# Performance work log

Measured on AMD Instinct MI355X. Metric: run time of the kernel, lower is better.

Reference implementation:

```python
import jax, jax.numpy as jnp
import numpy as np

N = 4096
D = 1024          # latent_vector_size
H, KD, VD = 16, 64, 64
MHK = H * KD      # 1024
MHV = H * VD      # 1024
HID = D // 2      # 512
EPS = 1e-5


def _layernorm(v, g, b):
    mu = jnp.mean(v, axis=-1, keepdims=True)
    var = jnp.mean(jnp.square(v - mu), axis=-1, keepdims=True)
    return (v - mu) * jax.lax.rsqrt(var + EPS) * g + b


def setup_inputs() -> dict:
    key = jax.random.key(0)
    ks = jax.random.split(key, 12)
    s = lambda fan_in: 1.0 / np.sqrt(fan_in)
    return {
        "x": jax.random.normal(ks[0], (N, D), dtype=jnp.float32),
        "w_qkv": jax.random.uniform(ks[1], (D, H * (2 * KD + VD)), jnp.float32, -s(D), s(D)),
        "b_qkv": jax.random.uniform(ks[2], (H * (2 * KD + VD),), jnp.float32, -s(D), s(D)),
        "w_msa": jax.random.uniform(ks[3], (MHV, D), jnp.float32, -s(MHV), s(MHV)),
        "b_msa": jax.random.uniform(ks[4], (D,), jnp.float32, -s(MHV), s(MHV)),
        "ln_g": jnp.ones((D,), jnp.float32),
        "ln_b": jnp.zeros((D,), jnp.float32),
        "w_h1": jax.random.uniform(ks[5], (D, HID), jnp.float32, -s(D), s(D)),
        "b_h1": jax.random.uniform(ks[6], (HID,), jnp.float32, -s(D), s(D)),
        "w_h2": jax.random.uniform(ks[7], (HID, D), jnp.float32, -s(HID), s(HID)),
        "b_h2": jax.random.uniform(ks[8], (D,), jnp.float32, -s(HID), s(HID)),
    }


def reference(x, w_qkv, b_qkv, w_msa, b_msa, ln_g, ln_b, w_h1, b_h1, w_h2, b_h2):
    # --- attention block (note: heads are never split; one big [N,N] softmax) ---
    ln1 = _layernorm(x, ln_g, ln_b)                       # [N, D]
    qkv = ln1 @ w_qkv + b_qkv                             # [N, 3*MHK]
    q, k, v = qkv[:, :MHK], qkv[:, MHK:2 * MHK], qkv[:, 2 * MHK:]
    scores = (q @ k.T) / jnp.sqrt(jnp.float32(KD))        # [N, N]
    attn = jax.nn.softmax(scores, axis=-1)
    mha = (attn @ v) @ w_msa + b_msa                      # [N, D]
    enc1 = x + mha
    # --- MLP block (shared layernorm params; softmax output, residual) ---
    ln2 = _layernorm(enc1, ln_g, ln_b)
    h1 = jax.nn.gelu(ln2 @ w_h1 + b_h1, approximate=False)  # [N, HID]
    h2 = jax.nn.gelu(h1 @ w_h2 + b_h2, approximate=False)   # [N, D]
    out = jax.nn.softmax(h2, axis=-1)                        # nn.Softmax() -> dim=1 for 2D
    return enc1 + out
```

## Files before the change

### kernel.cpp

```cpp
#include <hip/hip_runtime.h>
#include <stdint.h>

#define DEV __device__ __forceinline__

typedef unsigned short u16;
typedef __attribute__((ext_vector_type(8))) unsigned short u16x8;
typedef __attribute__((ext_vector_type(4))) unsigned short u16x4;
typedef __attribute__((ext_vector_type(4))) float f32x4;

DEV float bf2f(u16 u) { return __uint_as_float(((unsigned)u) << 16); }
DEV u16 f2bf(float f) {
  unsigned u = __float_as_uint(f);
  u += 0x7FFFu + ((u >> 16) & 1u);
  return (u16)(u >> 16);
}
DEV float gelu_exact(float v) { return 0.5f * v * (1.0f + erff(v * 0.70710678118654752f)); }

__global__ __launch_bounds__(256) void transpose_f32_bf16(
    const float* __restrict__ in, u16* __restrict__ out, int rows, int cols) {
  __shared__ float t[32][33];
  const int tx = threadIdx.x, ty = threadIdx.y;
  const int c0 = blockIdx.x * 32, r0 = blockIdx.y * 32;
#pragma unroll
  for (int i = 0; i < 32; i += 8) t[ty + i][tx] = in[(size_t)(r0 + ty + i) * cols + c0 + tx];
  __syncthreads();
#pragma unroll
  for (int i = 0; i < 32; i += 8)
    out[(size_t)(c0 + ty + i) * rows + r0 + tx] = f2bf(t[tx][ty + i]);
}

__global__ __launch_bounds__(256) void transpose_bf16(
    const u16* __restrict__ in, int ldin, u16* __restrict__ out, int ldout) {
  __shared__ u16 t[32][33];
  const int tx = threadIdx.x, ty = threadIdx.y;
  const int c0 = blockIdx.x * 32, r0 = blockIdx.y * 32;
#pragma unroll
  for (int i = 0; i < 32; i += 8) t[ty + i][tx] = in[(size_t)(r0 + ty + i) * ldin + c0 + tx];
  __syncthreads();
#pragma unroll
  for (int i = 0; i < 32; i += 8)
    out[(size_t)(c0 + ty + i) * ldout + r0 + tx] = t[tx][ty + i];
}

__global__ __launch_bounds__(256) void layernorm_bf16(
    const float* __restrict__ in, const float* __restrict__ g,
    const float* __restrict__ b, u16* __restrict__ out) {
  const int tid = threadIdx.x;
  const int lane = tid & 63, wid = tid >> 6;
  const size_t base = (size_t)blockIdx.x * 1024;
  const float4 v = ((const float4*)(in + base))[tid];
  float s = v.x + v.y + v.z + v.w;
  float ss = v.x * v.x + v.y * v.y + v.z * v.z + v.w * v.w;
#pragma unroll
  for (int off = 32; off > 0; off >>= 1) {
    s += __shfl_down(s, off);
    ss += __shfl_down(ss, off);
  }
  __shared__ float red[8];
  if (lane == 0) { red[wid] = s; red[4 + wid] = ss; }
  __syncthreads();
  s = red[0] + red[1] + red[2] + red[3];
  ss = red[4] + red[5] + red[6] + red[7];
  const float mu = s * (1.0f / 1024.0f);
  const float inv = rsqrtf(ss * (1.0f / 1024.0f) - mu * mu + 1e-5f);
  const float4 gv = ((const float4*)g)[tid];
  const float4 bv = ((const float4*)b)[tid];
  u16x4 o;
  o.x = f2bf((v.x - mu) * inv * gv.x + bv.x);
  o.y = f2bf((v.y - mu) * inv * gv.y + bv.y);
  o.z = f2bf((v.z - mu) * inv * gv.z + bv.z);
  o.w = f2bf((v.w - mu) * inv * gv.w + bv.w);
  *(u16x4*)(out + base + tid * 4) = o;
}

__global__ __launch_bounds__(256) void softmax4096(u16* __restrict__ p) {
  const int tid = threadIdx.x;
  const int lane = tid & 63, wid = tid >> 6;
  u16* row = p + (size_t)blockIdx.x * 4096;
  u16x8 r0 = ((u16x8*)row)[tid * 2];
  u16x8 r1 = ((u16x8*)row)[tid * 2 + 1];
  float v[16];
#pragma unroll
  for (int i = 0; i < 8; ++i) { v[i] = bf2f(r0[i]); v[8 + i] = bf2f(r1[i]); }
  float mx = v[0];
#pragma unroll
  for (int i = 1; i < 16; ++i) mx = fmaxf(mx, v[i]);
#pragma unroll
  for (int off = 32; off > 0; off >>= 1) mx = fmaxf(mx, __shfl_down(mx, off));
  __shared__ float red[8];
  if (lane == 0) red[wid] = mx;
  __syncthreads();
  mx = fmaxf(fmaxf(red[0], red[1]), fmaxf(red[2], red[3]));
  float sum = 0.0f;
#pragma unroll
  for (int i = 0; i < 16; ++i) { v[i] = __expf(v[i] - mx); sum += v[i]; }
#pragma unroll
  for (int off = 32; off > 0; off >>= 1) sum += __shfl_down(sum, off);
  if (lane == 0) red[4 + wid] = sum;
  __syncthreads();
  sum = red[4] + red[5] + red[6] + red[7];
  const float inv = 1.0f / sum;
  u16x8 o0, o1;
#pragma unroll
  for (int i = 0; i < 8; ++i) { o0[i] = f2bf(v[i] * inv); o1[i] = f2bf(v[8 + i] * inv); }
  ((u16x8*)row)[tid * 2] = o0;
  ((u16x8*)row)[tid * 2 + 1] = o1;
}

__global__ __launch_bounds__(256) void final_softmax_add(
    const float* __restrict__ h2, const float* __restrict__ enc1, float* __restrict__ out) {
  const int tid = threadIdx.x;
  const int lane = tid & 63, wid = tid >> 6;
  const size_t base = (size_t)blockIdx.x * 1024;
  float4 v = ((const float4*)(h2 + base))[tid];
  float mx = fmaxf(fmaxf(v.x, v.y), fmaxf(v.z, v.w));
#pragma unroll
  for (int off = 32; off > 0; off >>= 1) mx = fmaxf(mx, __shfl_down(mx, off));
  __shared__ float red[8];
  if (lane == 0) red[wid] = mx;
  __syncthreads();
  mx = fmaxf(fmaxf(red[0], red[1]), fmaxf(red[2], red[3]));
  v.x = __expf(v.x - mx); v.y = __expf(v.y - mx);
  v.z = __expf(v.z - mx); v.w = __expf(v.w - mx);
  float sum = v.x + v.y + v.z + v.w;
#pragma unroll
  for (int off = 32; off > 0; off >>= 1) sum += __shfl_down(sum, off);
  if (lane == 0) red[4 + wid] = sum;
  __syncthreads();
  sum = red[4] + red[5] + red[6] + red[7];
  const float inv = 1.0f / sum;
  const float4 e = ((const float4*)(enc1 + base))[tid];
  float4 o;
  o.x = e.x + v.x * inv; o.y = e.y + v.y * inv;
  o.z = e.z + v.z * inv; o.w = e.w + v.w * inv;
  ((float4*)(out + base))[tid] = o;
}

template <int EPI>
__global__ __launch_bounds__(256) void gemm_bt(
    const u16* __restrict__ A, int lda, const u16* __restrict__ Bt, int ldb,
    void* __restrict__ Cv, int ldc, const float* __restrict__ bias,
    const float* __restrict__ xres, int ldx, float scale, int K) {
  __shared__ alignas(16) u16 As[3][128 * 32];
  __shared__ alignas(16) u16 Bs[3][128 * 32];
  const int tid = threadIdx.x;
  const int wid = tid >> 6;
  const int lane = tid & 63;

  const int gx = gridDim.x;
  const int nwg = gridDim.x * gridDim.y;
  int wg = blockIdx.y * gx + blockIdx.x;
  wg = (wg & 7) * (nwg >> 3) + (wg >> 3);
  const int m0 = (wg / gx) * 128;
  const int n0 = (wg % gx) * 128;
  const int wr = wid >> 1, wc = wid & 1;

  const int srow = lane >> 2;
  const int sseg = (((lane & 3) ^ ((lane >> 3) & 3))) * 8;

  f32x4 acc[4][4];
#pragma unroll
  for (int m = 0; m < 4; ++m)
#pragma unroll
    for (int n = 0; n < 4; ++n) { f32x4 z = {0.f, 0.f, 0.f, 0.f}; acc[m][n] = z; }

  const int arow = wr * 64 + (lane & 15);
  const int brow = wc * 64 + (lane & 15);
  const int koff = (((lane >> 4) ^ ((lane >> 1) & 3))) * 8;

  const int NT = K >> 5;

  auto STAGE = [&](int kt, int buf) {
    const int k0 = kt * 32;
#pragma unroll
    for (int i = 0; i < 2; ++i) {
      const int r = i * 64 + wid * 16;
      const u16* ga = A + (size_t)(m0 + r + srow) * lda + k0 + sseg;
      const u16* gb = Bt + (size_t)(n0 + r + srow) * ldb + k0 + sseg;
      __builtin_amdgcn_global_load_lds((__attribute__((address_space(1))) void*)ga,
                                       (__attribute__((address_space(3))) void*)&As[buf][r * 32], 16, 0, 0);
      __builtin_amdgcn_global_load_lds((__attribute__((address_space(1))) void*)gb,
                                       (__attribute__((address_space(3))) void*)&Bs[buf][r * 32], 16, 0, 0);
    }
  };

  STAGE(0, 0);
  STAGE(1, 1);
  asm volatile("s_waitcnt vmcnt(4)" ::: "memory");
  __builtin_amdgcn_s_barrier();

  int cur = 0;
  for (int t = 0; t < NT; ++t) {
    const int kt = (t + 2 < NT) ? (t + 2) : (NT - 1);
    STAGE(kt, (cur + 2) % 3);

    u16x8 a[4], b[4];
#pragma unroll
    for (int m = 0; m < 4; ++m) a[m] = *(const u16x8*)&As[cur][(arow + m * 16) * 32 + koff];
#pragma unroll
    for (int n = 0; n < 4; ++n) b[n] = *(const u16x8*)&Bs[cur][(brow + n * 16) * 32 + koff];
#pragma unroll
    for (int m = 0; m < 4; ++m)
#pragma unroll
      for (int n = 0; n < 4; ++n)
        asm("v_mfma_f32_16x16x32_bf16 %0, %1, %2, %0" : "+v"(acc[m][n]) : "v"(a[m]), "v"(b[n]));

    asm volatile("s_waitcnt vmcnt(4)" ::: "memory");
    __builtin_amdgcn_s_barrier();
    cur = (cur + 1) % 3;
  }

  const int crow0 = m0 + wr * 64 + ((lane >> 4) << 2);
  const int ccol0 = n0 + wc * 64 + (lane & 15);
#pragma unroll
  for (int m = 0; m < 4; ++m) {
#pragma unroll
    for (int n = 0; n < 4; ++n) {
      const int col = ccol0 + n * 16;
      float bia = 0.0f;
      if (EPI == 1 || EPI == 3 || EPI == 4 || EPI == 5) bia = bias[col];
#pragma unroll
      for (int r = 0; r < 4; ++r) {
        const int row = crow0 + m * 16 + r;
        const float v = acc[m][n][r];
        if (EPI == 0) {
          ((u16*)Cv)[(size_t)row * ldc + col] = f2bf(v * scale);
        } else if (EPI == 1) {
          ((u16*)Cv)[(size_t)row * ldc + col] = f2bf(v + bia);
        } else if (EPI == 2) {
          ((u16*)Cv)[(size_t)row * ldc + col] = f2bf(v);
        } else if (EPI == 3) {
          ((float*)Cv)[(size_t)row * ldc + col] = v + bia + xres[(size_t)row * ldx + col];
        } else if (EPI == 4) {
          ((u16*)Cv)[(size_t)row * ldc + col] = f2bf(gelu_exact(v + bia));
        } else {
          ((float*)Cv)[(size_t)row * ldc + col] = gelu_exact(v + bia);
        }
      }
    }
  }
}

extern "C" void kernel_launch(void* const* d_in, const int* in_sizes, int n_in,
                              void* d_out, int out_size, void* d_ws, size_t ws_size,
                              hipStream_t stream) {
  const float* x     = (const float*)d_in[0];
  const float* w_qkv = (const float*)d_in[1];
  const float* b_qkv = (const float*)d_in[2];
  const float* w_msa = (const float*)d_in[3];
  const float* b_msa = (const float*)d_in[4];
  const float* ln_g  = (const float*)d_in[5];
  const float* ln_b  = (const float*)d_in[6];
  const float* w_h1  = (const float*)d_in[7];
  const float* b_h1  = (const float*)d_in[8];
  const float* w_h2  = (const float*)d_in[9];
  const float* b_h2  = (const float*)d_in[10];

  char* w = (char*)d_ws;
  u16*   qkv   = (u16*)(w + 0);
  u16*   sc    = (u16*)(w + 25165824);
  u16*   lnb   = (u16*)(w + 58720256);
  u16*   av    = (u16*)(w + 67108864);
  u16*   vT    = (u16*)(w + 75497472);
  float* enc1  = (float*)(w + 83886080);
  u16*   h1    = (u16*)(w + 100663296);
  float* h2    = (float*)(w + 104857600);
  u16*   wqkvT = (u16*)(w + 121634816);
  u16*   wmsaT = (u16*)(w + 127926272);
  u16*   wh1T  = (u16*)(w + 130023424);
  u16*   wh2T  = (u16*)(w + 131072000);
  (void)in_sizes; (void)n_in; (void)out_size; (void)ws_size;

  dim3 tb(32, 8);
  transpose_f32_bf16<<<dim3(96, 32), tb, 0, stream>>>(w_qkv, wqkvT, 1024, 3072);
  transpose_f32_bf16<<<dim3(32, 32), tb, 0, stream>>>(w_msa, wmsaT, 1024, 1024);
  transpose_f32_bf16<<<dim3(16, 32), tb, 0, stream>>>(w_h1, wh1T, 1024, 512);
  transpose_f32_bf16<<<dim3(32, 16), tb, 0, stream>>>(w_h2, wh2T, 512, 1024);

  layernorm_bf16<<<4096, 256, 0, stream>>>(x, ln_g, ln_b, lnb);
  gemm_bt<1><<<dim3(24, 32), 256, 0, stream>>>(lnb, 1024, wqkvT, 1024, qkv, 3072,
                                               b_qkv, nullptr, 0, 1.0f, 1024);
  transpose_bf16<<<dim3(32, 128), tb, 0, stream>>>(qkv + 2048, 3072, vT, 4096);
  gemm_bt<0><<<dim3(32, 32), 256, 0, stream>>>(qkv, 3072, qkv + 1024, 3072, sc, 4096,
                                               nullptr, nullptr, 0, 0.125f, 1024);
  softmax4096<<<4096, 256, 0, stream>>>(sc);
  gemm_bt<2><<<dim3(8, 32), 256, 0, stream>>>(sc, 4096, vT, 4096, av, 1024,
                                              nullptr, nullptr, 0, 1.0f, 4096);
  gemm_bt<3><<<dim3(8, 32), 256, 0, stream>>>(av, 1024, wmsaT, 1024, enc1, 1024,
                                              b_msa, x, 1024, 1.0f, 1024);
  layernorm_bf16<<<4096, 256, 0, stream>>>(enc1, ln_g, ln_b, lnb);
  gemm_bt<4><<<dim3(4, 32), 256, 0, stream>>>(lnb, 1024, wh1T, 1024, h1, 512,
                                              b_h1, nullptr, 0, 1.0f, 1024);
  gemm_bt<5><<<dim3(8, 32), 256, 0, stream>>>(h1, 512, wh2T, 512, h2, 1024,
                                              b_h2, nullptr, 0, 1.0f, 512);
  final_softmax_add<<<4096, 256, 0, stream>>>(h2, enc1, (float*)d_out);
}
```

Measured before the change: 282.5 us.

## Add 256x256 double-buffered GEMM kernel with split-K for attention GEMMs

Introduces a 512-thread 256x256-tile GEMM with 64-wide K steps, double-buffered LDS, interleaved staging and MFMA phases, and raised wave priority during MFMA. It is used for the QKV projection and QK^T score GEMMs, and with a 4-way split-K plus a separate bf16 partial-sum reduction kernel for the attention-times-V GEMM. The aim is more data reuse per tile and enough blocks for the long-K GEMM. In exchange, partial sums are rounded to bf16 before they are summed, and extra memory traffic is added for the partials.

Result: faster. 242.5 us (-14.1%).

```diff
diff --git a/kernel.cpp b/kernel.cpp
--- a/kernel.cpp
+++ b/kernel.cpp
@@ -15,6 +15,8 @@
   return (u16)(u >> 16);
 }
 DEV float gelu_exact(float v) { return 0.5f * v * (1.0f + erff(v * 0.70710678118654752f)); }
+
+#define BARF asm volatile("s_barrier" ::: "memory")
 
 __global__ __launch_bounds__(256) void transpose_f32_bf16(
     const float* __restrict__ in, u16* __restrict__ out, int rows, int cols) {
@@ -136,6 +138,175 @@
   ((float4*)(out + base))[tid] = o;
 }
 
+__global__ __launch_bounds__(256) void reduce_partials(
+    const u16* __restrict__ P, u16* __restrict__ out) {
+  const size_t i = ((size_t)blockIdx.x * 256 + threadIdx.x) * 8;
+  const size_t S = 4096ull * 1024ull;
+  u16x8 p0 = *(const u16x8*)(P + i);
+  u16x8 p1 = *(const u16x8*)(P + S + i);
+  u16x8 p2 = *(const u16x8*)(P + 2 * S + i);
+  u16x8 p3 = *(const u16x8*)(P + 3 * S + i);
+  u16x8 o;
+#pragma unroll
+  for (int j = 0; j < 8; ++j)
+    o[j] = f2bf(bf2f(p0[j]) + bf2f(p1[j]) + bf2f(p2[j]) + bf2f(p3[j]));
+  *(u16x8*)(out + i) = o;
+}
+
+template <int EPI>
+__global__ __launch_bounds__(512, 2) void gemm256(
+    const u16* __restrict__ A, int lda, const u16* __restrict__ Bt, int ldb,
+    u16* __restrict__ C, int ldc, const float* __restrict__ bias, float scale,
+    int K, int nsplit, size_t sliceStride) {
+  __shared__ alignas(16) u16 As[2][16384];
+  __shared__ alignas(16) u16 Bs[2][16384];
+  const int tid = threadIdx.x;
+  const int wid = tid >> 6;
+  const int lane = tid & 63;
+  const int wr = wid >> 2, wc = wid & 3;
+
+  const int gx = gridDim.x;
+  const int nwg = gx * gridDim.y;
+  int wg = blockIdx.y * gx + blockIdx.x;
+  wg = (wg & 7) * (nwg >> 3) + (wg >> 3);
+  const int by = wg / gx;
+  const int bxk = wg % gx;
+  const int ks = bxk % nsplit;
+  const int bx = bxk / nsplit;
+  const int m0 = by * 256, n0 = bx * 256;
+  A += (size_t)ks * K;
+  Bt += (size_t)ks * K;
+  C += (size_t)ks * sliceStride;
+
+  const u16* Apan = A + (size_t)m0 * lda;
+  const u16* Bpan = Bt + (size_t)n0 * ldb;
+
+  const int sgk = ((lane & 7) ^ ((lane >> 3) & 7)) * 8;
+  const int hi4 = lane >> 4;
+  const int kgo0 = ((0 * 4 + hi4) ^ (lane & 7)) * 8;
+  const int kgo1 = ((1 * 4 + hi4) ^ (lane & 7)) * 8;
+  const int arowo = (wr * 128 + (lane & 15)) * 64;
+  const int browo = (wc * 64 + (lane & 15)) * 64;
+
+  f32x4 acc[8][4];
+#pragma unroll
+  for (int m = 0; m < 8; ++m)
+#pragma unroll
+    for (int n = 0; n < 4; ++n) { f32x4 z = {0.f, 0.f, 0.f, 0.f}; acc[m][n] = z; }
+
+  u16x8 a[2][2], b[4][2];
+
+#define ST_HALF(dst, pan, ld, t, h)                                              \
+  {                                                                              \
+    _Pragma("unroll") for (int j = 0; j < 2; ++j) {                              \
+      const int chunk = (tid >> 6) * 2 + j;                                      \
+      const int row = (h)*128 + chunk * 8 + (lane >> 3);                         \
+      const u16* gsrc = (pan) + (size_t)row * (ld) + (t)*64 + sgk;               \
+      __builtin_amdgcn_global_load_lds(                                          \
+          (const __attribute__((address_space(1))) void*)gsrc,                   \
+          (__attribute__((address_space(3))) void*)((dst) + (h)*8192 +           \
+                                                    chunk * 512 + lane * 8),     \
+          16, 0, 0);                                                             \
+    }                                                                            \
+  }
+
+#define LOADB(S)                                                                 \
+  _Pragma("unroll") for (int n = 0; n < 4; ++n) {                                \
+    b[n][0] = *(const u16x8*)&Bs[S][browo + n * 1024 + kgo0];                    \
+    b[n][1] = *(const u16x8*)&Bs[S][browo + n * 1024 + kgo1];                    \
+  }
+
+#define LOADA(S, Q)                                                              \
+  _Pragma("unroll") for (int mi = 0; mi < 2; ++mi) {                             \
+    a[mi][0] = *(const u16x8*)&As[S][arowo + (2 * (Q) + mi) * 1024 + kgo0];      \
+    a[mi][1] = *(const u16x8*)&As[S][arowo + (2 * (Q) + mi) * 1024 + kgo1];      \
+  }
+
+#define MMQ(Q)                                                                   \
+  BARF;                                                                          \
+  asm volatile("s_waitcnt lgkmcnt(0)" ::: "memory");                             \
+  __builtin_amdgcn_sched_barrier(0);                                             \
+  __builtin_amdgcn_s_setprio(1);                                                 \
+  _Pragma("unroll") for (int mi = 0; mi < 2; ++mi)                               \
+      _Pragma("unroll") for (int n = 0; n < 4; ++n)                              \
+          _Pragma("unroll") for (int kk = 0; kk < 2; ++kk)                       \
+              asm("v_mfma_f32_16x16x32_bf16 %0, %1, %2, %0"                      \
+                  : "+v"(acc[2 * ((Q) & 3) + mi][n])                             \
+                  : "v"(a[mi][kk]), "v"(b[n][kk]));                              \
+  __builtin_amdgcn_s_setprio(0);
+
+#define VMW asm volatile("s_waitcnt vmcnt(4)" ::: "memory");
+
+  const int NT = K >> 6;
+  const int NI = NT >> 1;
+
+  ST_HALF(&Bs[0][0], Bpan, ldb, 0, 0);
+  ST_HALF(&Bs[0][0], Bpan, ldb, 0, 1);
+  ST_HALF(&As[0][0], Apan, lda, 0, 0);
+  ST_HALF(&As[0][0], Apan, lda, 0, 1);
+  ST_HALF(&Bs[1][0], Bpan, ldb, 1, 0);
+  ST_HALF(&Bs[1][0], Bpan, ldb, 1, 1);
+  VMW;
+  BARF;
+
+  for (int it = 0; it < NI; ++it) {
+    const int t0 = 2 * it, t1 = t0 + 1;
+    const int tS0 = (t0 + 2 < NT) ? t0 + 2 : NT - 1;
+    const int tS1 = (t1 + 2 < NT) ? t1 + 2 : NT - 1;
+    LOADB(0); LOADA(0, 0);
+    ST_HALF(&As[1][0], Apan, lda, t1, 0);
+    ST_HALF(&As[1][0], Apan, lda, t1, 1);
+    MMQ(0); BARF;
+    LOADA(0, 1);
+    ST_HALF(&Bs[0][0], Bpan, ldb, tS0, 0);
+    MMQ(1); BARF;
+    LOADA(0, 2);
+    ST_HALF(&Bs[0][0], Bpan, ldb, tS0, 1);
+    MMQ(2); BARF;
+    LOADA(0, 3);
+    MMQ(3); VMW; BARF;
+    LOADB(1); LOADA(1, 0);
+    ST_HALF(&As[0][0], Apan, lda, tS0, 0);
+    ST_HALF(&As[0][0], Apan, lda, tS0, 1);
+    MMQ(4); BARF;
+    LOADA(1, 1);
+    ST_HALF(&Bs[1][0], Bpan, ldb, tS1, 0);
+    MMQ(5); BARF;
+    LOADA(1, 2);
+    ST_HALF(&Bs[1][0], Bpan, ldb, tS1, 1);
+    MMQ(6); BARF;
+    LOADA(1, 3);
+    MMQ(7); VMW; BARF;
+  }
+  asm volatile("s_waitcnt vmcnt(0)" ::: "memory");
+  BARF;
+
+  const int crow0 = m0 + wr * 128 + hi4 * 4;
+  const int ccol0 = n0 + wc * 64 + (lane & 15);
+#pragma unroll
+  for (int m = 0; m < 8; ++m) {
+#pragma unroll
+    for (int n = 0; n < 4; ++n) {
+      const int col = ccol0 + n * 16;
+      float bia = 0.0f;
+      if (EPI == 1) bia = bias[col];
+#pragma unroll
+      for (int r = 0; r < 4; ++r) {
+        const int row = crow0 + m * 16 + r;
+        float v = acc[m][n][r];
+        if (EPI == 0) v *= scale;
+        if (EPI == 1) v += bia;
+        C[(size_t)row * ldc + col] = f2bf(v);
+      }
+    }
+  }
+#undef ST_HALF
+#undef LOADB
+#undef LOADA
+#undef MMQ
+#undef VMW
+}
+
 template <int EPI>
 __global__ __launch_bounds__(256) void gemm_bt(
     const u16* __restrict__ A, int lda, const u16* __restrict__ Bt, int ldb,
@@ -177,9 +348,9 @@
       const int r = i * 64 + wid * 16;
       const u16* ga = A + (size_t)(m0 + r + srow) * lda + k0 + sseg;
       const u16* gb = Bt + (size_t)(n0 + r + srow) * ldb + k0 + sseg;
-      __builtin_amdgcn_global_load_lds((__attribute__((address_space(1))) void*)ga,
+      __builtin_amdgcn_global_load_lds((const __attribute__((address_space(1))) void*)ga,
                                        (__attribute__((address_space(3))) void*)&As[buf][r * 32], 16, 0, 0);
-      __builtin_amdgcn_global_load_lds((__attribute__((address_space(1))) void*)gb,
+      __builtin_amdgcn_global_load_lds((const __attribute__((address_space(1))) void*)gb,
                                        (__attribute__((address_space(3))) void*)&Bs[buf][r * 32], 16, 0, 0);
     }
   };
@@ -187,7 +358,7 @@
   STAGE(0, 0);
   STAGE(1, 1);
   asm volatile("s_waitcnt vmcnt(4)" ::: "memory");
-  __builtin_amdgcn_s_barrier();
+  BARF;
 
   int cur = 0;
   for (int t = 0; t < NT; ++t) {
@@ -199,6 +370,8 @@
     for (int m = 0; m < 4; ++m) a[m] = *(const u16x8*)&As[cur][(arow + m * 16) * 32 + koff];
 #pragma unroll
     for (int n = 0; n < 4; ++n) b[n] = *(const u16x8*)&Bs[cur][(brow + n * 16) * 32 + koff];
+    asm volatile("s_waitcnt lgkmcnt(0)" ::: "memory");
+    __builtin_amdgcn_sched_barrier(0);
 #pragma unroll
     for (int m = 0; m < 4; ++m)
 #pragma unroll
@@ -206,7 +379,7 @@
         asm("v_mfma_f32_16x16x32_bf16 %0, %1, %2, %0" : "+v"(acc[m][n]) : "v"(a[m]), "v"(b[n]));
 
     asm volatile("s_waitcnt vmcnt(4)" ::: "memory");
-    __builtin_amdgcn_s_barrier();
+    BARF;
     cur = (cur + 1) % 3;
   }
 
@@ -218,18 +391,12 @@
     for (int n = 0; n < 4; ++n) {
       const int col = ccol0 + n * 16;
       float bia = 0.0f;
-      if (EPI == 1 || EPI == 3 || EPI == 4 || EPI == 5) bia = bias[col];
+      if (EPI == 3 || EPI == 4 || EPI == 5) bia = bias[col];
 #pragma unroll
       for (int r = 0; r < 4; ++r) {
         const int row = crow0 + m * 16 + r;
         const float v = acc[m][n][r];
-        if (EPI == 0) {
-          ((u16*)Cv)[(size_t)row * ldc + col] = f2bf(v * scale);
-        } else if (EPI == 1) {
-          ((u16*)Cv)[(size_t)row * ldc + col] = f2bf(v + bia);
-        } else if (EPI == 2) {
-          ((u16*)Cv)[(size_t)row * ldc + col] = f2bf(v);
-        } else if (EPI == 3) {
+        if (EPI == 3) {
           ((float*)Cv)[(size_t)row * ldc + col] = v + bia + xres[(size_t)row * ldx + col];
         } else if (EPI == 4) {
           ((u16*)Cv)[(size_t)row * ldc + col] = f2bf(gelu_exact(v + bia));
@@ -263,6 +430,7 @@
   u16*   av    = (u16*)(w + 67108864);
   u16*   vT    = (u16*)(w + 75497472);
   float* enc1  = (float*)(w + 83886080);
+  u16*   part  = (u16*)(w + 83886080);
   u16*   h1    = (u16*)(w + 100663296);
   float* h2    = (float*)(w + 104857600);
   u16*   wqkvT = (u16*)(w + 121634816);
@@ -278,14 +446,15 @@
   transpose_f32_bf16<<<dim3(32, 16), tb, 0, stream>>>(w_h2, wh2T, 512, 1024);
 
   layernorm_bf16<<<4096, 256, 0, stream>>>(x, ln_g, ln_b, lnb);
-  gemm_bt<1><<<dim3(24, 32), 256, 0, stream>>>(lnb, 1024, wqkvT, 1024, qkv, 3072,
-                                               b_qkv, nullptr, 0, 1.0f, 1024);
+  gemm256<1><<<dim3(12, 16), 512, 0, stream>>>(lnb, 1024, wqkvT, 1024, qkv, 3072,
+                                               b_qkv, 1.0f, 1024, 1, 0);
   transpose_bf16<<<dim3(32, 128), tb, 0, stream>>>(qkv + 2048, 3072, vT, 4096);
-  gemm_bt<0><<<dim3(32, 32), 256, 0, stream>>>(qkv, 3072, qkv + 1024, 3072, sc, 4096,
-                                               nullptr, nullptr, 0, 0.125f, 1024);
+  gemm256<0><<<dim3(16, 16), 512, 0, stream>>>(qkv, 3072, qkv + 1024, 3072, sc, 4096,
+                                               nullptr, 0.125f, 1024, 1, 0);
   softmax4096<<<4096, 256, 0, stream>>>(sc);
-  gemm_bt<2><<<dim3(8, 32), 256, 0, stream>>>(sc, 4096, vT, 4096, av, 1024,
-                                              nullptr, nullptr, 0, 1.0f, 4096);
+  gemm256<2><<<dim3(16, 16), 512, 0, stream>>>(sc, 4096, vT, 4096, part, 1024,
+                                               nullptr, 1.0f, 1024, 4, 4096ull * 1024ull);
+  reduce_partials<<<2048, 256, 0, stream>>>(part, av);
   gemm_bt<3><<<dim3(8, 32), 256, 0, stream>>>(av, 1024, wmsaT, 1024, enc1, 1024,
                                               b_msa, x, 1024, 1.0f, 1024);
   layernorm_bf16<<<4096, 256, 0, stream>>>(enc1, ln_g, ln_b, lnb);
```
